# Performance work log

Measured on AMD Instinct MI355X. Metric: run time of the kernel, lower is better.

Reference implementation:

```python
import jax, jax.numpy as jnp
import numpy as np


def setup_inputs() -> dict:
    key = jax.random.key(0)
    ks = jax.random.split(key, 8)
    T, D = 8192, 36
    return {
        "embeddings": jax.random.normal(ks[0], (T, D), dtype=jnp.float32),
        "WQ_prog": jax.random.normal(ks[1], (2, D), dtype=jnp.float32),
        "WK_prog": jax.random.normal(ks[2], (2, D), dtype=jnp.float32),
        "WV_op": jax.random.normal(ks[3], (1, D), dtype=jnp.float32),
        "WV_arg": jax.random.normal(ks[4], (1, D), dtype=jnp.float32),
        "WQ_stack": jax.random.normal(ks[5], (2, D), dtype=jnp.float32),
        "WK_stack": jax.random.normal(ks[6], (2, D), dtype=jnp.float32),
        "WV_stack": jax.random.normal(ks[7], (1, D), dtype=jnp.float32),
    }


def reference(embeddings, WQ_prog, WK_prog, WV_op, WV_arg, WQ_stack, WK_stack, WV_stack):
    # --- program-fetch head: hard-argmax attention ---
    Q_prog = embeddings @ WQ_prog.T          # (T, 2)
    K_prog = embeddings @ WK_prog.T          # (T, 2)
    V_op = embeddings @ WV_op.T              # (T, 1)
    V_arg = embeddings @ WV_arg.T            # (T, 1)
    scores_prog = Q_prog @ K_prog.T          # (T, T)
    best_prog = jnp.argmax(scores_prog, axis=1)   # (T,)
    fetched_ops = V_op[best_prog, 0]
    fetched_args = V_arg[best_prog, 0]

    # --- stack-fetch head: hard-argmax attention ---
    Q_stack = embeddings @ WQ_stack.T        # (T, 2)
    K_stack = embeddings @ WK_stack.T        # (T, 2)
    V_stack = embeddings @ WV_stack.T        # (T, 1)
    scores_stack = Q_stack @ K_stack.T       # (T, T)
    best_stack = jnp.argmax(scores_stack, axis=1)
    fetched_vals = V_stack[best_stack, 0]

    return (fetched_ops, fetched_args, fetched_vals)
```

## Files before the change

kernel.cpp:

```cpp
#include <hip/hip_runtime.h>
#include <math.h>

#define T 8192
#define D 36
#define NCH 16
#define CHUNK (T / NCH)
#define RPT (CHUNK / 256)


__device__ __forceinline__ void load_row(const float* __restrict__ E, int j,
                                         float* e) {
    const float4* Er = (const float4*)(E + j * D);
#pragma unroll
    for (int i = 0; i < D / 4; ++i) {
        float4 v = Er[i];
        e[4 * i + 0] = v.x;
        e[4 * i + 1] = v.y;
        e[4 * i + 2] = v.z;
        e[4 * i + 3] = v.w;
    }
}

__global__ __launch_bounds__(256) void maxscan_kernel(
    const float* __restrict__ E,
    const float* __restrict__ WQp, const float* __restrict__ WKp,
    const float* __restrict__ WQs, const float* __restrict__ WKs,
    float* __restrict__ pv, float2* __restrict__ Kg, float2* __restrict__ Qg) {
    const int head = blockIdx.z;
    const float* __restrict__ WQ = head ? WQs : WQp;
    const float* __restrict__ WK = head ? WKs : WKp;

    __shared__ float2 sk[CHUNK];
    const int j0 = blockIdx.y * CHUNK;

#pragma unroll
    for (int r = 0; r < RPT; ++r) {
        const int j = j0 + r * 256 + threadIdx.x;
        float e[D];
        load_row(E, j, e);
        float k0 = 0.f, k1 = 0.f;
#pragma unroll
        for (int d = 0; d < D; ++d) {
            k0 = fmaf(e[d], WK[d], k0);
            k1 = fmaf(e[d], WK[D + d], k1);
        }
        float2 kk = make_float2(k0, k1);
        sk[r * 256 + threadIdx.x] = kk;
        if (blockIdx.x == 0) Kg[head * T + j] = kk;
    }

    const int row = blockIdx.x * 256 + threadIdx.x;
    float q0 = 0.f, q1 = 0.f;
    {
        float e[D];
        load_row(E, row, e);
#pragma unroll
        for (int d = 0; d < D; ++d) {
            q0 = fmaf(e[d], WQ[d], q0);
            q1 = fmaf(e[d], WQ[D + d], q1);
        }
    }
    if (blockIdx.y == 0) Qg[head * T + row] = make_float2(q0, q1);
    __syncthreads();

    float best = -INFINITY;
    const float4* sk4 = (const float4*)sk;
#pragma unroll 8
    for (int k = 0; k < CHUNK / 2; ++k) {
        float4 kk = sk4[k];
        float s0 = fmaf(q0, kk.x, q1 * kk.y);
        float s1 = fmaf(q0, kk.z, q1 * kk.w);
        best = fmaxf(best, fmaxf(s0, s1));
    }
    pv[blockIdx.y * 2 * T + head * T + row] = best;
}

__global__ __launch_bounds__(256) void finalize_wave(
    const float* __restrict__ E,
    const float* __restrict__ WVop, const float* __restrict__ WVarg,
    const float* __restrict__ WVs,
    const float* __restrict__ pv, const float2* __restrict__ Kg,
    const float2* __restrict__ Qg, float* __restrict__ out) {
    const int wid = threadIdx.x >> 6;
    const int lane = threadIdx.x & 63;
    const int prow = blockIdx.x * 4 + wid;
    const int head = prow >> 13;
    const int row = prow & (T - 1);

    const float v = (lane < NCH) ? pv[lane * 2 * T + prow] : -INFINITY;
    float m = v;
#pragma unroll
    for (int off = 8; off; off >>= 1) m = fmaxf(m, __shfl_xor(m, off));
    m = __shfl(m, 0);

    const unsigned long long cb = __ballot(v == m);
    const int cwin = __ffsll(cb) - 1;

    const float2 q = Qg[prow];
    int bi = 0;
#pragma unroll 1
    for (int i = 0; i < CHUNK / 64; ++i) {
        const int j = cwin * CHUNK + i * 64 + lane;
        const float2 kk = Kg[head * T + j];
        const float s = fmaf(q.x, kk.x, q.y * kk.y);
        const unsigned long long eb = __ballot(s == m);
        if (eb) {
            bi = cwin * CHUNK + i * 64 + __ffsll(eb) - 1;
            break;
        }
    }

    float e[D];
    load_row(E, bi, e);
    if (head == 0) {
        float vop = 0.f, varg = 0.f;
#pragma unroll
        for (int d = 0; d < D; ++d) {
            vop = fmaf(e[d], WVop[d], vop);
            varg = fmaf(e[d], WVarg[d], varg);
        }
        if (lane == 0) {
            out[row] = vop;
            out[T + row] = varg;
        }
    } else {
        float vs = 0.f;
#pragma unroll
        for (int d = 0; d < D; ++d) vs = fmaf(e[d], WVs[d], vs);
        if (lane == 0) out[2 * T + row] = vs;
    }
}

extern "C" void kernel_launch(void* const* d_in, const int* in_sizes, int n_in,
                              void* d_out, int out_size, void* d_ws,
                              size_t ws_size, hipStream_t stream) {
    const float* E = (const float*)d_in[0];
    const float* WQp = (const float*)d_in[1];
    const float* WKp = (const float*)d_in[2];
    const float* WVop = (const float*)d_in[3];
    const float* WVarg = (const float*)d_in[4];
    const float* WQs = (const float*)d_in[5];
    const float* WKs = (const float*)d_in[6];
    const float* WVs = (const float*)d_in[7];
    float* out = (float*)d_out;

    float* wsf = (float*)d_ws;
    float* pv = wsf;
    float2* Kg = (float2*)(wsf + 2 * T * NCH);
    float2* Qg = (float2*)(wsf + 2 * T * NCH + 4 * T);

    dim3 gA(T / 256, NCH, 2);
    maxscan_kernel<<<gA, 256, 0, stream>>>(E, WQp, WKp, WQs, WKs, pv, Kg, Qg);

    finalize_wave<<<(2 * T) / 4, 256, 0, stream>>>(E, WVop, WVarg, WVs, pv, Kg,
                                                   Qg, out);
}
```

Measured before the change: 112.1 us.

## Split Q/K projection into its own kernel and register-tile max scan over rows

Moves the Q/K projections into a separate kernel that computes all four projections once per row, so the scan kernel no longer recomputes K for every chunk and row-block. The max-scan kernel now gives each thread 8 query rows that reuse each shared K entry, with 64 chunks of 128 keys instead of 16 chunks of 512. Finalize reduces over all 64 lanes and checks at most two 64-key windows. This adds a third kernel launch, a larger partial-max buffer, and fewer blocks in the scan grid (4x64x2).

New measurement: 94.31 us (median of 2 runs). 15.9% less time.

```diff
diff --git a/kernel.cpp b/kernel.cpp
--- a/kernel.cpp
+++ b/kernel.cpp
@@ -3,9 +3,11 @@
 
 #define T 8192
 #define D 36
-#define NCH 16
+#define NCH 64
 #define CHUNK (T / NCH)
-#define RPT (CHUNK / 256)
+#define RPT 8
+#define ROWS_PER_BLOCK (256 * RPT)
+#define RBLK (T / ROWS_PER_BLOCK)
 
 
 __device__ __forceinline__ void load_row(const float* __restrict__ E, int j,
@@ -21,92 +23,103 @@
     }
 }
 
-__global__ __launch_bounds__(256) void maxscan_kernel(
+__global__ __launch_bounds__(256) void proj_qk(
     const float* __restrict__ E,
     const float* __restrict__ WQp, const float* __restrict__ WKp,
     const float* __restrict__ WQs, const float* __restrict__ WKs,
-    float* __restrict__ pv, float2* __restrict__ Kg, float2* __restrict__ Qg) {
+    float2* __restrict__ Qg, float2* __restrict__ Kg) {
+    const int t = blockIdx.x * 256 + threadIdx.x;
+    float e[D];
+    load_row(E, t, e);
+    float qp0 = 0.f, qp1 = 0.f, kp0 = 0.f, kp1 = 0.f;
+    float qs0 = 0.f, qs1 = 0.f, ks0 = 0.f, ks1 = 0.f;
+#pragma unroll
+    for (int d = 0; d < D; ++d) {
+        float ed = e[d];
+        qp0 = fmaf(ed, WQp[d], qp0);
+        qp1 = fmaf(ed, WQp[D + d], qp1);
+        kp0 = fmaf(ed, WKp[d], kp0);
+        kp1 = fmaf(ed, WKp[D + d], kp1);
+        qs0 = fmaf(ed, WQs[d], qs0);
+        qs1 = fmaf(ed, WQs[D + d], qs1);
+        ks0 = fmaf(ed, WKs[d], ks0);
+        ks1 = fmaf(ed, WKs[D + d], ks1);
+    }
+    Qg[t] = make_float2(qp0, qp1);
+    Qg[T + t] = make_float2(qs0, qs1);
+    Kg[t] = make_float2(kp0, kp1);
+    Kg[T + t] = make_float2(ks0, ks1);
+}
+
+__global__ __launch_bounds__(256) void maxscan(
+    const float2* __restrict__ Qg, const float2* __restrict__ Kg,
+    float* __restrict__ pv) {
     const int head = blockIdx.z;
-    const float* __restrict__ WQ = head ? WQs : WQp;
-    const float* __restrict__ WK = head ? WKs : WKp;
-
-    __shared__ float2 sk[CHUNK];
+    const int row0 = blockIdx.x * ROWS_PER_BLOCK;
     const int j0 = blockIdx.y * CHUNK;
 
+    __shared__ float4 sk4[CHUNK / 2];
+    if (threadIdx.x < CHUNK)
+        ((float2*)sk4)[threadIdx.x] = Kg[head * T + j0 + threadIdx.x];
+
+    float2 q[RPT];
 #pragma unroll
-    for (int r = 0; r < RPT; ++r) {
-        const int j = j0 + r * 256 + threadIdx.x;
-        float e[D];
-        load_row(E, j, e);
-        float k0 = 0.f, k1 = 0.f;
-#pragma unroll
-        for (int d = 0; d < D; ++d) {
-            k0 = fmaf(e[d], WK[d], k0);
-            k1 = fmaf(e[d], WK[D + d], k1);
-        }
-        float2 kk = make_float2(k0, k1);
-        sk[r * 256 + threadIdx.x] = kk;
-        if (blockIdx.x == 0) Kg[head * T + j] = kk;
-    }
-
-    const int row = blockIdx.x * 256 + threadIdx.x;
-    float q0 = 0.f, q1 = 0.f;
-    {
-        float e[D];
-        load_row(E, row, e);
-#pragma unroll
-        for (int d = 0; d < D; ++d) {
-            q0 = fmaf(e[d], WQ[d], q0);
-            q1 = fmaf(e[d], WQ[D + d], q1);
-        }
-    }
-    if (blockIdx.y == 0) Qg[head * T + row] = make_float2(q0, q1);
+    for (int i = 0; i < RPT; ++i)
+        q[i] = Qg[head * T + row0 + i * 256 + threadIdx.x];
     __syncthreads();
 
-    float best = -INFINITY;
-    const float4* sk4 = (const float4*)sk;
+    float best[RPT];
+#pragma unroll
+    for (int i = 0; i < RPT; ++i) best[i] = -INFINITY;
+
 #pragma unroll 8
     for (int k = 0; k < CHUNK / 2; ++k) {
         float4 kk = sk4[k];
-        float s0 = fmaf(q0, kk.x, q1 * kk.y);
-        float s1 = fmaf(q0, kk.z, q1 * kk.w);
-        best = fmaxf(best, fmaxf(s0, s1));
+#pragma unroll
+        for (int i = 0; i < RPT; ++i) {
+            float s0 = fmaf(q[i].x, kk.x, q[i].y * kk.y);
+            float s1 = fmaf(q[i].x, kk.z, q[i].y * kk.w);
+            best[i] = fmaxf(best[i], fmaxf(s0, s1));
+        }
     }
-    pv[blockIdx.y * 2 * T + head * T + row] = best;
+    const int base = blockIdx.y * 2 * T + head * T + row0 + threadIdx.x;
+#pragma unroll
+    for (int i = 0; i < RPT; ++i) pv[base + i * 256] = best[i];
 }
 
-__global__ __launch_bounds__(256) void finalize_wave(
+__global__ __launch_bounds__(256) void finalize(
     const float* __restrict__ E,
     const float* __restrict__ WVop, const float* __restrict__ WVarg,
     const float* __restrict__ WVs,
-    const float* __restrict__ pv, const float2* __restrict__ Kg,
-    const float2* __restrict__ Qg, float* __restrict__ out) {
+    const float* __restrict__ pv, const float2* __restrict__ Qg,
+    const float2* __restrict__ Kg, float* __restrict__ out) {
     const int wid = threadIdx.x >> 6;
     const int lane = threadIdx.x & 63;
     const int prow = blockIdx.x * 4 + wid;
     const int head = prow >> 13;
     const int row = prow & (T - 1);
 
-    const float v = (lane < NCH) ? pv[lane * 2 * T + prow] : -INFINITY;
+    const float v = pv[lane * 2 * T + prow];
     float m = v;
 #pragma unroll
-    for (int off = 8; off; off >>= 1) m = fmaxf(m, __shfl_xor(m, off));
-    m = __shfl(m, 0);
-
+    for (int off = 32; off; off >>= 1) m = fmaxf(m, __shfl_xor(m, off));
     const unsigned long long cb = __ballot(v == m);
     const int cwin = __ffsll(cb) - 1;
 
     const float2 q = Qg[prow];
-    int bi = 0;
-#pragma unroll 1
-    for (int i = 0; i < CHUNK / 64; ++i) {
-        const int j = cwin * CHUNK + i * 64 + lane;
-        const float2 kk = Kg[head * T + j];
-        const float s = fmaf(q.x, kk.x, q.y * kk.y);
-        const unsigned long long eb = __ballot(s == m);
+    int bi;
+    {
+        int j = head * T + cwin * CHUNK + lane;
+        float2 kk = Kg[j];
+        float s = fmaf(q.x, kk.x, q.y * kk.y);
+        unsigned long long eb = __ballot(s == m);
         if (eb) {
-            bi = cwin * CHUNK + i * 64 + __ffsll(eb) - 1;
-            break;
+            bi = cwin * CHUNK + __ffsll(eb) - 1;
+        } else {
+            kk = Kg[j + 64];
+            s = fmaf(q.x, kk.x, q.y * kk.y);
+            eb = __ballot(s == m);
+            bi = cwin * CHUNK + 64 + __ffsll(eb) - 1;
         }
     }
 
@@ -149,9 +162,11 @@
     float2* Kg = (float2*)(wsf + 2 * T * NCH);
     float2* Qg = (float2*)(wsf + 2 * T * NCH + 4 * T);
 
-    dim3 gA(T / 256, NCH, 2);
-    maxscan_kernel<<<gA, 256, 0, stream>>>(E, WQp, WKp, WQs, WKs, pv, Kg, Qg);
+    proj_qk<<<T / 256, 256, 0, stream>>>(E, WQp, WKp, WQs, WKs, Qg, Kg);
 
-    finalize_wave<<<(2 * T) / 4, 256, 0, stream>>>(E, WVop, WVarg, WVs, pv, Kg,
-                                                   Qg, out);
+    dim3 gB(RBLK, NCH, 2);
+    maxscan<<<gB, 256, 0, stream>>>(Qg, Kg, pv);
+
+    finalize<<<(2 * T) / 4, 256, 0, stream>>>(E, WVop, WVarg, WVs, pv, Qg, Kg,
+                                              out);
 }
```
